# Performance work log

Hardware: AMD Instinct MI355X
Metric: run time of the kernel (lower is better)

Reference implementation:

```python
import jax, jax.numpy as jnp
import numpy as np

EPS = 1e-12  # torch F.normalize eps


def unfold(x, ksize, pad):
    # torch F.unfold equivalent: [B,C,H,W] -> [B, C*k*k, L], channel-major ordering
    patches = jax.lax.conv_general_dilated_patches(
        x, (ksize, ksize), (1, 1), [(pad, pad), (pad, pad)],
        dimension_numbers=('NCHW', 'OIHW', 'NCHW'))
    B, CKK, Hp, Wp = patches.shape
    return patches.reshape(B, CKK, Hp * Wp)


def fold(patches, C, ksize, H, W, pad):
    # torch F.fold equivalent (stride 1): overlap-add of [B, C*k*k, H*W] -> [B,C,H,W]
    B = patches.shape[0]
    p = patches.reshape(B, C, ksize, ksize, H, W)
    out = jnp.zeros((B, C, H + 2 * pad, W + 2 * pad), patches.dtype)
    for di in range(ksize):
        for dj in range(ksize):
            out = out.at[:, :, di:di + H, dj:dj + W].add(p[:, :, di, dj])
    return out[:, :, pad:pad + H, pad:pad + W]


def setup_inputs() -> dict:
    key = jax.random.key(0)
    ks = jax.random.split(key, 4)
    B, C, H, W = 2, 512, 64, 64
    D, CIN = 256, 512 * 9  # embed: Linear(tdim*8*3*3 -> tdim*4), tdim=64
    return {
        'query': jax.random.normal(ks[0], (B, C, H, W), dtype=jnp.float32),
        'key': jax.random.normal(ks[1], (B, C, H, W), dtype=jnp.float32),
        'value': jax.random.normal(ks[2], (B, C, H, W), dtype=jnp.float32),
        'W_embed': jax.random.normal(ks[3], (D, CIN), dtype=jnp.float32) * 0.02,
        'k': 3,
    }


def reference(query, key, value, W_embed, k):
    B, Cv, H, W = value.shape
    # patch embed: unfold -> linear (no bias)
    q_unf = unfold(query, k, k // 2)                       # [B, C*k*k, L]
    k_unf = unfold(key, k, k // 2)                         # [B, C*k*k, L]
    k_emb = jnp.einsum('bcl,dc->bld', k_unf, W_embed)      # [B, L, D]
    q_emb = jnp.einsum('bcl,dc->bdl', q_unf, W_embed)      # [B, D, L]
    # cosine correlation
    k_n = k_emb / jnp.maximum(jnp.linalg.norm(k_emb, axis=2, keepdims=True), EPS)
    q_n = q_emb / jnp.maximum(jnp.linalg.norm(q_emb, axis=1, keepdims=True), EPS)
    corr = jnp.einsum('bld,bdm->blm', k_n, q_n)            # [B, L_key, L_query]
    corr_value = jnp.max(corr, axis=1)                     # [B, L]
    corr_argmax = jnp.argmax(corr, axis=1)                 # [B, L]
    # swap(V=value, idx=corr_argmax, s=1, k=k)
    s = 1
    temph = s * k + H * s - H - s                          # = k - 1
    tempw = s * k + W * s - W - s
    ph = max(temph // 2 + temph % 2, 1)
    pw = max(tempw // 2 + tempw % 2, 1)
    v_unf = unfold(value, k, ph)                           # [B, Cv*k*k, L] (ph==pw for square)
    t_unf = jnp.take_along_axis(v_unf, corr_argmax[:, None, :], axis=2)
    divisor = fold(jnp.ones_like(t_unf), Cv, k, H, W, ph)
    T = fold(t_unf, Cv, k, H, W, ph) / divisor             # [B, Cv, H, W]
    S = corr_value.reshape(B, 1, H, W)
    return S, T
```

## Files before the change

kernel.cpp:

```cpp
#include <hip/hip_runtime.h>
#include <hip/hip_bf16.h>
#include <stdint.h>
#include <math.h>

#define BB 2
#define CC 512
#define HH 64
#define WW 64
#define LL 4096
#define DD 256
#define CIN 4608
#define NG 144

typedef _Float16 half_t;
typedef __attribute__((ext_vector_type(8))) _Float16 f16x8;
typedef __attribute__((ext_vector_type(4))) _Float16 f16x4;
typedef __attribute__((ext_vector_type(4))) float f32x4;

__global__ __launch_bounds__(256) void presplit(const float* __restrict__ query,
                                                const float* __restrict__ key,
                                                char* __restrict__ img_ts) {
    __shared__ float tile[32][65];
    int img = blockIdx.y;
    int y   = blockIdx.x;
    const float* src = ((img >> 1) ? key : query) + (size_t)(img & 1) * CC * LL + y * WW;
    char* dstbase = img_ts + ((size_t)img * 64 + y) * (16 * 64 * 128);
    int t = threadIdx.x;
    int xl = t & 63, c4 = t >> 6;
    int xw = t >> 2, fsw = t & 3;
    for (int cc = 0; cc < 16; ++cc) {
#pragma unroll
        for (int j = 0; j < 8; ++j) {
            int cl = c4 + j * 4;
            tile[cl][xl] = src[(size_t)(cc * 32 + cl) * LL + xl];
        }
        __syncthreads();
        f16x8 h8, l8;
#pragma unroll
        for (int j = 0; j < 8; ++j) {
            float v = tile[fsw * 8 + j][xw];
            half_t h = (half_t)v;
            h8[j] = h; l8[j] = (half_t)(v - (float)h);
        }
        char* p = dstbase + (size_t)cc * 8192 + xw * 128;
        int swz = (xw & 7) << 4;
        *(f16x8*)(p + ((fsw * 16) ^ swz)) = h8;
        *(f16x8*)(p + ((64 + fsw * 16) ^ swz)) = l8;
        __syncthreads();
    }
}

__global__ __launch_bounds__(256) void splitW2b(const float* __restrict__ W,
                                                char* __restrict__ Wst) {
    int i = blockIdx.x * 256 + threadIdx.x;
    if (i >= NG * DD * 4) return;
    int g  = i >> 10;
    int r  = i & 1023;
    int d  = r >> 2;
    int fs = r & 3;
    int cc = g / 9, o = g - cc * 9;
    const float* src = W + (size_t)d * CIN;
    f16x8 h8, l8;
#pragma unroll
    for (int j = 0; j < 8; j++) {
        float w = src[(cc * 32 + fs * 8 + j) * 9 + o];
        half_t h = (half_t)w;
        h8[j] = h;
        l8[j] = (half_t)(w - (float)h);
    }
    size_t base = (size_t)g * 32768 + d * 128;
    int sw = (d & 7) << 4;
    *(f16x8*)(Wst + base + ((fs * 16) ^ sw)) = h8;
    *(f16x8*)(Wst + base + ((64 + fs * 16) ^ sw)) = l8;
}

__global__ __launch_bounds__(512, 2) void embed_mfma(const char* __restrict__ img_ts,
                                                     const char* __restrict__ Wst,
                                                     const char* __restrict__ zp,
                                                     float* __restrict__ part) {
    __shared__ char sW[2][32768];
    __shared__ char sB[2][33792];

    int iid = blockIdx.y;
    int ks  = blockIdx.z;
    int lt  = blockIdx.x;
    int y0  = lt * 2;
    int t = threadIdx.x;
    int w = t >> 6, lane = t & 63;
    int fr = lane & 15, fs = lane >> 4;

    const char* imgb = img_ts + (size_t)iid * (64 * 16 * 64 * 128) + (size_t)ks * 65536;
    const char *ps0, *ps1, *ps2, *ps3, *ps4;
    int pb0, pb1, pb2, pb3, pb4;
#define PREP(qv, PS, PB)                                                \
    {                                                                   \
        int q = (qv);                                                   \
        int ri = q / 528;                                               \
        int rem = q - ri * 528;                                         \
        int xi = rem >> 3, sub = rem & 7;                               \
        int xg = xi - 1, yg = y0 - 1 + ri;                              \
        bool ok = (yg >= 0) && (yg < 64) && (xg >= 0) && (xg < 64);     \
        PS = ok ? imgb + (size_t)yg * 131072 + (size_t)xg * 128 + sub * 16 \
                : zp + ((q & 255) * 16);                                \
        PB = ok ? 8192 : 0;                                             \
    }
    PREP(t, ps0, pb0); PREP(512 + t, ps1, pb1); PREP(1024 + t, ps2, pb2);
    PREP(1536 + t, ps3, pb3); PREP(2048 + t, ps4, pb4);

    const char* pWl = Wst + (size_t)ks * 72 * 32768 + (w << 12) + lane * 16;
    char* wdst0 = &sW[0][0] + (w << 12) + lane * 16;
    char* wdst1 = wdst0 + 32768;
    char* bB0 = &sB[0][0] + t * 16;

    int swzA = (fr & 7) << 4;
    const char* aBH = &sW[0][0] + (w << 12) + fr * 128 + ((fs * 16) ^ swzA);
    const char* aBL = &sW[0][0] + (w << 12) + fr * 128 + ((64 + fs * 16) ^ swzA);
    const char* bH0 = &sB[0][0] + (fr + 0) * 128 + ((fs * 16) ^ (((fr - 1) & 7) << 4));
    const char* bL0 = &sB[0][0] + (fr + 0) * 128 + (((64 + fs * 16)) ^ (((fr - 1) & 7) << 4));
    const char* bH1 = &sB[0][0] + (fr + 1) * 128 + ((fs * 16) ^ (((fr) & 7) << 4));
    const char* bL1 = &sB[0][0] + (fr + 1) * 128 + (((64 + fs * 16)) ^ (((fr) & 7) << 4));
    const char* bH2 = &sB[0][0] + (fr + 2) * 128 + ((fs * 16) ^ (((fr + 1) & 7) << 4));
    const char* bL2 = &sB[0][0] + (fr + 2) * 128 + (((64 + fs * 16)) ^ (((fr + 1) & 7) << 4));

#define GLL(src, dst)                                                   \
    __builtin_amdgcn_global_load_lds(                                   \
        (const __attribute__((address_space(1))) void*)(src),           \
        (__attribute__((address_space(3))) void*)(dst), 16, 0, 0)

#define DMAW(SEL)                                                       \
    do {                                                                \
        char* wd_ = (SEL) ? wdst1 : wdst0;                              \
        GLL(pWl, wd_);                                                  \
        GLL(pWl + 1024, wd_ + 1024);                                    \
        GLL(pWl + 2048, wd_ + 2048);                                    \
        GLL(pWl + 3072, wd_ + 3072);                                    \
        pWl += 32768;                                                   \
    } while (0)

#define DMAB(SEL)                                                       \
    do {                                                                \
        char* bd_ = bB0 + (SEL) * 33792;                                \
        GLL(ps0, bd_);                                                  \
        GLL(ps1, bd_ + 8192);                                           \
        GLL(ps2, bd_ + 16384);                                          \
        GLL(ps3, bd_ + 24576);                                          \
        if (t < 64) GLL(ps4, bd_ + 32768);                              \
        ps0 += pb0; ps1 += pb1; ps2 += pb2; ps3 += pb3; ps4 += pb4;     \
    } while (0)

#define RDA(AH, AL, BSEL)                                               \
    do {                                                                \
        AH[0] = *(const f16x8*)(aBH + (BSEL) * 32768);                  \
        AL[0] = *(const f16x8*)(aBL + (BSEL) * 32768);                  \
        AH[1] = *(const f16x8*)(aBH + 2048 + (BSEL) * 32768);           \
        AL[1] = *(const f16x8*)(aBL + 2048 + (BSEL) * 32768);           \
    } while (0)

#define RDB(DI, DJ, CSEL)                                               \
    do {                                                                \
        const char* h_ = (DJ) == 0 ? bH0 : (DJ) == 1 ? bH1 : bH2;       \
        const char* l_ = (DJ) == 0 ? bL0 : (DJ) == 1 ? bL1 : bL2;       \
        _Pragma("unroll")                                               \
        for (int cg = 0; cg < 8; cg++) {                                \
            int imm = ((cg >> 2) + (DI)) * 8448 + (cg & 3) * 2048 + (CSEL) * 33792; \
            bh[cg] = *(const f16x8*)(h_ + imm);                         \
            bl[cg] = *(const f16x8*)(l_ + imm);                         \
        }                                                               \
    } while (0)

#define DOMFMA(AH, AL)                                                  \
    do {                                                                \
        _Pragma("unroll")                                               \
        for (int rg = 0; rg < 2; rg++)                                  \
            _Pragma("unroll")                                           \
            for (int cg = 0; cg < 8; cg++)                              \
                acc[rg][cg] = __builtin_amdgcn_mfma_f32_16x16x32_f16(AH[rg], bh[cg], acc[rg][cg], 0, 0, 0); \
        _Pragma("unroll")                                               \
        for (int rg = 0; rg < 2; rg++)                                  \
            _Pragma("unroll")                                           \
            for (int cg = 0; cg < 8; cg++) {                            \
                acc[rg][cg] = __builtin_amdgcn_mfma_f32_16x16x32_f16(AH[rg], bl[cg], acc[rg][cg], 0, 0, 0); \
                acc[rg][cg] = __builtin_amdgcn_mfma_f32_16x16x32_f16(AL[rg], bh[cg], acc[rg][cg], 0, 0, 0); \
            }                                                           \
    } while (0)

    f32x4 acc[2][8];
#pragma unroll
    for (int rg = 0; rg < 2; rg++)
#pragma unroll
        for (int cg = 0; cg < 8; cg++) acc[rg][cg] = (f32x4){0.f, 0.f, 0.f, 0.f};

    f16x8 ah0[2], al0[2], ah1[2], al1[2];
    f16x8 bh[8], bl[8];

    DMAB(0);
    DMAW(0);
    DMAW(1);
    asm volatile("s_waitcnt vmcnt(4)" ::: "memory");
    __builtin_amdgcn_sched_barrier(0);
    RDA(ah0, al0, 0);
    __builtin_amdgcn_sched_barrier(0);

#define BODY(KK, O, CSEL, NSEL, DI, DJ)                                 \
    do {                                                                \
        if ((O) == 0) __builtin_amdgcn_s_barrier();                     \
        asm volatile("s_waitcnt lgkmcnt(0)" ::: "memory");              \
        __builtin_amdgcn_sched_barrier(0);                              \
        DMAW((KK) & 1);                                                 \
        if ((O) == 1) DMAB(NSEL);                                       \
        if ((O) == 1 || (O) == 2)                                       \
            asm volatile("s_waitcnt vmcnt(8)" ::: "memory");            \
        else                                                            \
            asm volatile("s_waitcnt vmcnt(4)" ::: "memory");            \
        __builtin_amdgcn_sched_barrier(0);                              \
        if ((KK) & 1) { RDA(ah0, al0, ((KK) + 1) & 1); }                \
        else          { RDA(ah1, al1, ((KK) + 1) & 1); }                \
        RDB(DI, DJ, CSEL);                                              \
        __builtin_amdgcn_sched_barrier(0);                              \
        if ((KK) & 1) DOMFMA(ah1, al1); else DOMFMA(ah0, al0);          \
    } while (0)

#pragma unroll 1
    for (int cp = 0; cp < 4; ++cp) {
        BODY(0, 0, 0, 1, 0, 0);  BODY(1, 1, 0, 1, 0, 1);  BODY(2, 2, 0, 1, 0, 2);
        BODY(3, 3, 0, 1, 1, 0);  BODY(4, 4, 0, 1, 1, 1);  BODY(5, 5, 0, 1, 1, 2);
        BODY(6, 6, 0, 1, 2, 0);  BODY(7, 7, 0, 1, 2, 1);  BODY(8, 8, 0, 1, 2, 2);
        BODY(9, 0, 1, 0, 0, 0);  BODY(10, 1, 1, 0, 0, 1); BODY(11, 2, 1, 0, 0, 2);
        BODY(12, 3, 1, 0, 1, 0); BODY(13, 4, 1, 0, 1, 1); BODY(14, 5, 1, 0, 1, 2);
        BODY(15, 6, 1, 0, 2, 0); BODY(16, 7, 1, 0, 2, 1); BODY(17, 8, 1, 0, 2, 2);
    }
#undef BODY

    float* pt = part + (((size_t)iid * 32 + lt) * 2 + ks) * 32768;
#pragma unroll
    for (int rg = 0; rg < 2; rg++)
#pragma unroll
        for (int cg = 0; cg < 8; cg++) {
            int l = cg * 16 + fr;
            int d0 = w * 32 + rg * 16 + fs * 4;
#pragma unroll
            for (int r = 0; r < 4; r++)
                pt[(d0 + r) * 128 + l] = acc[rg][cg][r];
        }
#undef PREP
#undef GLL
#undef DMAW
#undef DMAB
#undef RDA
#undef RDB
#undef DOMFMA
}

__global__ __launch_bounds__(256) void norm_split(const float* __restrict__ part,
                                                  char* __restrict__ qemb,
                                                  char* __restrict__ kemb) {
    __shared__ float sm[4][64];
    __shared__ float invn[64];
    __shared__ char stage[64][1040];

    int iid = blockIdx.y;
    int bx  = blockIdx.x;
    int lt  = bx >> 1, lh2 = bx & 1;
    const float* p0 = part + (((size_t)iid * 32 + lt) * 2 + 0) * 32768 + lh2 * 64;
    const float* p1 = p0 + 32768;
    int t = threadIdx.x;
    int ll = t & 63, dq = t >> 6;

    float v[64];
    float sq = 0.f;
#pragma unroll
    for (int dd = 0; dd < 64; ++dd) {
        int d = dq * 64 + dd;
        float x = p0[d * 128 + ll] + p1[d * 128 + ll];
        v[dd] = x;
        sq += x * x;
    }
    sm[dq][ll] = sq;
    __syncthreads();
    if (t < 64) {
        float s = sm[0][t] + sm[1][t] + sm[2][t] + sm[3][t];
        invn[t] = 1.0f / fmaxf(sqrtf(s), 1e-12f);
    }
    __syncthreads();

    float sc = invn[ll];
    int swb = (ll & 7) << 4;
#pragma unroll
    for (int oc = 0; oc < 8; ++oc) {
        int d0 = dq * 64 + oc * 8;
        f16x8 h8, l8;
#pragma unroll
        for (int j = 0; j < 8; ++j) {
            float x = v[oc * 8 + j] * sc;
            half_t h = (half_t)x;
            h8[j] = h;
            l8[j] = (half_t)(x - (float)h);
        }
        int itb = d0 >> 5;
        int fsc = (d0 >> 3) & 3;
        *(f16x8*)&stage[ll][itb * 128 + ((fsc * 16) ^ swb)] = h8;
        *(f16x8*)&stage[ll][itb * 128 + ((64 + fsc * 16) ^ swb)] = l8;
    }
    __syncthreads();

    int b = iid & 1, type = iid >> 1;
    char* e = (type ? kemb : qemb);
    int rr = t >> 2, c0 = t & 3;
    char* erow = e + ((size_t)b * LL + lt * 128 + lh2 * 64 + rr) * 1024;
    const char* srow = &stage[rr][0];
#pragma unroll
    for (int c = 0; c < 16; ++c) {
        int cj = c0 + c * 4;
        *(float4*)(erow + cj * 16) = *(const float4*)(srow + cj * 16);
    }
}

__global__ void init_packed(unsigned long long* p, int n) {
    int i = blockIdx.x * 256 + threadIdx.x;
    if (i < n) p[i] = 0ull;
}

__global__ __launch_bounds__(256, 2) void corr_max_mfma(const char* __restrict__ kemb,
                                                        const char* __restrict__ qemb,
                                                        unsigned long long* __restrict__ packed) {
    __shared__ char sA[2][16384];
    __shared__ char sBq[2][16384];

    int b  = blockIdx.z;
    int l0 = blockIdx.y * 128;
    int m0 = blockIdx.x * 128;
    int t  = threadIdx.x;
    int w = t >> 6, lane = t & 63;
    int wr = w >> 1, wc = w & 1;
    int fr = lane & 15, fs = lane >> 4;

    const char* Abase = kemb + ((size_t)b * LL + l0) * 1024;
    const char* Bbase = qemb + ((size_t)b * LL + m0) * 1024;

    f32x4 acc[4][4];
#pragma unroll
    for (int i = 0; i < 4; i++)
#pragma unroll
        for (int j = 0; j < 4; j++) acc[i][j] = (f32x4){0.f, 0.f, 0.f, 0.f};

#define DMA2(bufi, itv)                                                   \
    do {                                                                  \
        _Pragma("unroll")                                                 \
        for (int c = 0; c < 4; c++) {                                     \
            int idx = c * 4096 + t * 16;                                  \
            int row = idx >> 7, offb = idx & 127;                         \
            __builtin_amdgcn_global_load_lds(                             \
                (const __attribute__((address_space(1))) void*)(Abase + (size_t)row * 1024 + (itv) * 128 + offb), \
                (__attribute__((address_space(3))) void*)(&sA[bufi][idx]), 16, 0, 0); \
        }                                                                 \
        _Pragma("unroll")                                                 \
        for (int c = 0; c < 4; c++) {                                     \
            int idx = c * 4096 + t * 16;                                  \
            int row = idx >> 7, offb = idx & 127;                         \
            __builtin_amdgcn_global_load_lds(                             \
                (const __attribute__((address_space(1))) void*)(Bbase + (size_t)row * 1024 + (itv) * 128 + offb), \
                (__attribute__((address_space(3))) void*)(&sBq[bufi][idx]), 16, 0, 0); \
        }                                                                 \
    } while (0)

    DMA2(0, 0);

    f16x8 ah[4], al[4], bh[4], bl[4];
    for (int it = 0; it < 8; ++it) {
        asm volatile("s_waitcnt vmcnt(0) lgkmcnt(0)" ::: "memory");
        __builtin_amdgcn_s_barrier();
        __builtin_amdgcn_sched_barrier(0);
        if (it < 7) DMA2((it + 1) & 1, it + 1);
        __builtin_amdgcn_sched_barrier(0);
        const char* sa = sA[it & 1];
        const char* sb = sBq[it & 1];
#pragma unroll
        for (int rg = 0; rg < 4; rg++) {
            int r = wr * 64 + rg * 16 + fr;
            const char* rp = sa + r * 128;
            int sw_ = (r & 7) << 4;
            ah[rg] = *(const f16x8*)(rp + ((fs * 16) ^ sw_));
            al[rg] = *(const f16x8*)(rp + ((64 + fs * 16) ^ sw_));
        }
#pragma unroll
        for (int cg = 0; cg < 4; cg++) {
            int r = wc * 64 + cg * 16 + fr;
            const char* rp = sb + r * 128;
            int sw_ = (r & 7) << 4;
            bh[cg] = *(const f16x8*)(rp + ((fs * 16) ^ sw_));
            bl[cg] = *(const f16x8*)(rp + ((64 + fs * 16) ^ sw_));
        }
#pragma unroll
        for (int rg = 0; rg < 4; rg++)
#pragma unroll
            for (int cg = 0; cg < 4; cg++)
                acc[rg][cg] = __builtin_amdgcn_mfma_f32_16x16x32_f16(ah[rg], bh[cg], acc[rg][cg], 0, 0, 0);
#pragma unroll
        for (int rg = 0; rg < 4; rg++)
#pragma unroll
            for (int cg = 0; cg < 4; cg++) {
                acc[rg][cg] = __builtin_amdgcn_mfma_f32_16x16x32_f16(ah[rg], bl[cg], acc[rg][cg], 0, 0, 0);
                acc[rg][cg] = __builtin_amdgcn_mfma_f32_16x16x32_f16(al[rg], bh[cg], acc[rg][cg], 0, 0, 0);
            }
    }
#undef DMA2

#pragma unroll
    for (int cg = 0; cg < 4; cg++) {
        unsigned long long best = 0ull;
#pragma unroll
        for (int rg = 0; rg < 4; rg++) {
#pragma unroll
            for (int r = 0; r < 4; r++) {
                unsigned u = __float_as_uint(acc[rg][cg][r]);
                u = (u & 0x80000000u) ? ~u : (u | 0x80000000u);
                int l = l0 + wr * 64 + rg * 16 + fs * 4 + r;
                unsigned long long p = ((unsigned long long)u << 32) | (unsigned)(4095 - l);
                best = (p > best) ? p : best;
            }
        }
        unsigned long long oo;
        oo = __shfl_xor(best, 16); best = (oo > best) ? oo : best;
        oo = __shfl_xor(best, 32); best = (oo > best) ? oo : best;
        if (lane < 16)
            atomicMax(&packed[(size_t)b * LL + m0 + wc * 64 + cg * 16 + lane], best);
    }
}

__global__ void decode_packed(const unsigned long long* __restrict__ packed,
                              float* __restrict__ S_out, int* __restrict__ arg) {
    int i = blockIdx.x * 256 + threadIdx.x;
    if (i < BB * LL) {
        unsigned long long p = packed[i];
        unsigned u = (unsigned)(p >> 32);
        unsigned bits = (u & 0x80000000u) ? (u & 0x7FFFFFFFu) : ~u;
        S_out[i] = __uint_as_float(bits);
        arg[i] = 4095 - (int)(unsigned)(p & 0xFFFFFFFFull);
    }
}

__global__ __launch_bounds__(256) void transpose_mat(const float* __restrict__ src,
                                                     float* __restrict__ dst,
                                                     int R, int Cc) {
    __shared__ float tile[32][33];
    size_t boff = (size_t)blockIdx.z * R * Cc;
    int bx = blockIdx.x;
    int by = blockIdx.y;
    int tx = threadIdx.x & 31;
    int ty = threadIdx.x >> 5;
    const float* s = src + boff;
    float* d = dst + boff;
#pragma unroll
    for (int i = 0; i < 4; i++) {
        int r = by * 32 + ty + i * 8;
        int c = bx * 32 + tx;
        tile[ty + i * 8][tx] = s[(size_t)r * Cc + c];
    }
    __syncthreads();
#pragma unroll
    for (int i = 0; i < 4; i++) {
        int c = bx * 32 + ty + i * 8;
        int r = by * 32 + tx;
        d[(size_t)c * R + r] = tile[tx][ty + i * 8];
    }
}

__global__ __launch_bounds__(256) void gather_fold(const float* __restrict__ value_t,
                                                   const int* __restrict__ arg,
                                                   float* __restrict__ T_t) {
    int b = blockIdx.y;
    int pix = blockIdx.x;
    int y = pix >> 6, x = pix & 63;
    int t = threadIdx.x;
    float2 acc = make_float2(0.f, 0.f);
    int cnty = (y == 0 || y == HH - 1) ? 2 : 3;
    int cntx = (x == 0 || x == WW - 1) ? 2 : 3;
    const int* ab = arg + b * LL;
    const float* vb = value_t + (size_t)b * LL * CC;
#pragma unroll
    for (int di = 0; di < 3; di++) {
        int my = y + 1 - di;
        if (my < 0 || my >= HH) continue;
#pragma unroll
        for (int dj = 0; dj < 3; dj++) {
            int mx = x + 1 - dj;
            if (mx < 0 || mx >= WW) continue;
            int a = ab[my * WW + mx];
            int ay = a >> 6, ax = a & 63;
            int vy = ay + di - 1, vx = ax + dj - 1;
            if (vy < 0 || vy >= HH || vx < 0 || vx >= WW) continue;
            float2 v = *(const float2*)&vb[((size_t)(vy * WW + vx)) * CC + t * 2];
            acc.x += v.x; acc.y += v.y;
        }
    }
    float inv = 1.0f / (float)(cnty * cntx);
    acc.x *= inv; acc.y *= inv;
    *(float2*)&T_t[((size_t)b * LL + pix) * CC + t * 2] = acc;
}

extern "C" void kernel_launch(void* const* d_in, const int* in_sizes, int n_in,
                              void* d_out, int out_size, void* d_ws, size_t ws_size,
                              hipStream_t stream) {
    const float* query = (const float*)d_in[0];
    const float* key   = (const float*)d_in[1];
    const float* value = (const float*)d_in[2];
    const float* Wemb  = (const float*)d_in[3];

    float* out   = (float*)d_out;
    float* S_out = out;
    float* T_out = out + BB * LL;

    char* ws = (char*)d_ws;
    char*  img_ts = ws;
    char*  Wst    = ws + 33554432;
    float* part   = (float*)(ws + 38273024);
    char*  qemb   = ws + 71827456;
    char*  kemb   = ws + 80216064;
    unsigned long long* packed = (unsigned long long*)(ws + 88604672);
    char*  zp     = ws + 88670208;
    int*   arg    = (int*)(ws + 88674304);
    float* val_t  = (float*)(ws + 38273024);
    float* T_t    = (float*)(ws + 38273024 + 16777216);

    init_packed   <<<dim3(34), 256, 0, stream>>>(packed, 8704);
    presplit      <<<dim3(64, 4), 256, 0, stream>>>(query, key, img_ts);
    splitW2b      <<<dim3(576), 256, 0, stream>>>(Wemb, Wst);
    embed_mfma    <<<dim3(32, 4, 2), 512, 0, stream>>>(img_ts, Wst, zp, part);
    norm_split    <<<dim3(64, 4), 256, 0, stream>>>(part, qemb, kemb);
    corr_max_mfma <<<dim3(32, 32, 2), 256, 0, stream>>>(kemb, qemb, packed);
    decode_packed <<<dim3(32), 256, 0, stream>>>(packed, S_out, arg);
    transpose_mat <<<dim3(128, 16, 2), 256, 0, stream>>>(value, val_t, CC, LL);
    gather_fold   <<<dim3(4096, 2), 256, 0, stream>>>(val_t, arg, T_t);
    transpose_mat <<<dim3(16, 128, 2), 256, 0, stream>>>(T_t, T_out, LL, CC);
}
```

Before: 208.5 us.

## Double-buffer B fragments and prefetch LDS reads one step ahead of MFMA

Splits the B-fragment registers into two sets and restructures the GEMM loop so each step issues its MFMAs first, then reads the next step's A/B fragments from LDS and issues the next global-to-LDS DMA. A prologue preloads two steps, and the per-iteration barrier moves to a different step with new wait counts. The goal is to hide LDS read latency behind MFMA work and to remove the full lgkmcnt(0) stall at the start of every step. The cost is doubled B-fragment register use, which may lower occupancy or cause spills. The reworked barrier and vmcnt placement also risks read-before-write hazards on the shared buffers.

```diff
diff --git a/kernel.cpp b/kernel.cpp
--- a/kernel.cpp
+++ b/kernel.cpp
@@ -156,31 +156,31 @@
         AL[1] = *(const f16x8*)(aBL + 2048 + (BSEL) * 32768);           \
     } while (0)
 
-#define RDB(DI, DJ, CSEL)                                               \
+#define RDB(BH, BL, DI, DJ, CSEL)                                       \
     do {                                                                \
         const char* h_ = (DJ) == 0 ? bH0 : (DJ) == 1 ? bH1 : bH2;       \
         const char* l_ = (DJ) == 0 ? bL0 : (DJ) == 1 ? bL1 : bL2;       \
         _Pragma("unroll")                                               \
         for (int cg = 0; cg < 8; cg++) {                                \
             int imm = ((cg >> 2) + (DI)) * 8448 + (cg & 3) * 2048 + (CSEL) * 33792; \
-            bh[cg] = *(const f16x8*)(h_ + imm);                         \
-            bl[cg] = *(const f16x8*)(l_ + imm);                         \
+            BH[cg] = *(const f16x8*)(h_ + imm);                         \
+            BL[cg] = *(const f16x8*)(l_ + imm);                         \
         }                                                               \
     } while (0)
 
-#define DOMFMA(AH, AL)                                                  \
+#define DOMFMA(AH, AL, BH, BL)                                          \
     do {                                                                \
         _Pragma("unroll")                                               \
         for (int rg = 0; rg < 2; rg++)                                  \
             _Pragma("unroll")                                           \
             for (int cg = 0; cg < 8; cg++)                              \
-                acc[rg][cg] = __builtin_amdgcn_mfma_f32_16x16x32_f16(AH[rg], bh[cg], acc[rg][cg], 0, 0, 0); \
+                acc[rg][cg] = __builtin_amdgcn_mfma_f32_16x16x32_f16(AH[rg], BH[cg], acc[rg][cg], 0, 0, 0); \
         _Pragma("unroll")                                               \
         for (int rg = 0; rg < 2; rg++)                                  \
             _Pragma("unroll")                                           \
             for (int cg = 0; cg < 8; cg++) {                            \
-                acc[rg][cg] = __builtin_amdgcn_mfma_f32_16x16x32_f16(AH[rg], bl[cg], acc[rg][cg], 0, 0, 0); \
-                acc[rg][cg] = __builtin_amdgcn_mfma_f32_16x16x32_f16(AL[rg], bh[cg], acc[rg][cg], 0, 0, 0); \
+                acc[rg][cg] = __builtin_amdgcn_mfma_f32_16x16x32_f16(AH[rg], BL[cg], acc[rg][cg], 0, 0, 0); \
+                acc[rg][cg] = __builtin_amdgcn_mfma_f32_16x16x32_f16(AL[rg], BH[cg], acc[rg][cg], 0, 0, 0); \
             }                                                           \
     } while (0)
 
@@ -191,43 +191,70 @@
         for (int cg = 0; cg < 8; cg++) acc[rg][cg] = (f32x4){0.f, 0.f, 0.f, 0.f};
 
     f16x8 ah0[2], al0[2], ah1[2], al1[2];
-    f16x8 bh[8], bl[8];
+    f16x8 bh0[8], bl0[8], bh1[8], bl1[8];
 
     DMAB(0);
     DMAW(0);
     DMAW(1);
     asm volatile("s_waitcnt vmcnt(4)" ::: "memory");
     __builtin_amdgcn_sched_barrier(0);
+    __builtin_amdgcn_s_barrier();
+    __builtin_amdgcn_sched_barrier(0);
     RDA(ah0, al0, 0);
     __builtin_amdgcn_sched_barrier(0);
-
-#define BODY(KK, O, CSEL, NSEL, DI, DJ)                                 \
+    RDB(bh0, bl0, 0, 0, 0);
+    asm volatile("s_waitcnt lgkmcnt(15)" ::: "memory");
+    __builtin_amdgcn_sched_barrier(0);
+    DMAW(0);
+    asm volatile("s_waitcnt vmcnt(4)" ::: "memory");
+    __builtin_amdgcn_sched_barrier(0);
+    RDA(ah1, al1, 1);
+    __builtin_amdgcn_sched_barrier(0);
+    RDB(bh1, bl1, 0, 1, 0);
+    asm volatile("s_waitcnt lgkmcnt(15)" ::: "memory");
+    __builtin_amdgcn_sched_barrier(0);
+    DMAW(1);
+
+#define BODY(KK, O, CSEL2, DI2, DJ2, V8)                                \
     do {                                                                \
-        if ((O) == 0) __builtin_amdgcn_s_barrier();                     \
-        asm volatile("s_waitcnt lgkmcnt(0)" ::: "memory");              \
-        __builtin_amdgcn_sched_barrier(0);                              \
-        DMAW((KK) & 1);                                                 \
-        if ((O) == 1) DMAB(NSEL);                                       \
-        if ((O) == 1 || (O) == 2)                                       \
+        if ((O) == 7) {                                                 \
+            asm volatile("s_waitcnt lgkmcnt(0)" ::: "memory");          \
+            __builtin_amdgcn_s_barrier();                               \
+            __builtin_amdgcn_sched_barrier(0);                          \
+        }                                                               \
+        if ((KK) >= 15)                                                 \
+            asm volatile("s_waitcnt vmcnt(0)" ::: "memory");            \
+        else if (V8)                                                    \
             asm volatile("s_waitcnt vmcnt(8)" ::: "memory");            \
         else                                                            \
             asm volatile("s_waitcnt vmcnt(4)" ::: "memory");            \
         __builtin_amdgcn_sched_barrier(0);                              \
-        if ((KK) & 1) { RDA(ah0, al0, ((KK) + 1) & 1); }                \
-        else          { RDA(ah1, al1, ((KK) + 1) & 1); }                \
-        RDB(DI, DJ, CSEL);                                              \
+        if ((KK) & 1) DOMFMA(ah1, al1, bh1, bl1);                       \
+        else          DOMFMA(ah0, al0, bh0, bl0);                       \
         __builtin_amdgcn_sched_barrier(0);                              \
-        if ((KK) & 1) DOMFMA(ah1, al1); else DOMFMA(ah0, al0);          \
+        if (cp < 3 || (KK) < 16) {                                      \
+            if ((KK) & 1) { RDA(ah1, al1, (KK) & 1);                    \
+                            __builtin_amdgcn_sched_barrier(0);          \
+                            RDB(bh1, bl1, DI2, DJ2, CSEL2); }           \
+            else          { RDA(ah0, al0, (KK) & 1);                    \
+                            __builtin_amdgcn_sched_barrier(0);          \
+                            RDB(bh0, bl0, DI2, DJ2, CSEL2); }           \
+        }                                                               \
+        asm volatile("s_waitcnt lgkmcnt(15)" ::: "memory");             \
+        __builtin_amdgcn_sched_barrier(0);                              \
+        if (cp < 3 || (KK) < 14) DMAW((KK) & 1);                        \
+        if ((O) == 1) { if ((KK) == 1 || cp < 3) DMAB(((KK) == 1) ? 1 : 0); } \
+        __builtin_amdgcn_sched_barrier(0);                              \
     } while (0)
 
 #pragma unroll 1
     for (int cp = 0; cp < 4; ++cp) {
-        BODY(0, 0, 0, 1, 0, 0);  BODY(1, 1, 0, 1, 0, 1);  BODY(2, 2, 0, 1, 0, 2);
-        BODY(3, 3, 0, 1, 1, 0);  BODY(4, 4, 0, 1, 1, 1);  BODY(5, 5, 0, 1, 1, 2);
-        BODY(6, 6, 0, 1, 2, 0);  BODY(7, 7, 0, 1, 2, 1);  BODY(8, 8, 0, 1, 2, 2);
-        BODY(9, 0, 1, 0, 0, 0);  BODY(10, 1, 1, 0, 0, 1); BODY(11, 2, 1, 0, 0, 2);
-        BODY(12, 3, 1, 0, 1, 0); BODY(13, 4, 1, 0, 1, 1); BODY(14, 5, 1, 0, 1, 2);
-        BODY(15, 6, 1, 0, 2, 0); BODY(16, 7, 1, 0, 2, 1); BODY(17, 8, 1, 0, 2, 2);
+        BODY(0, 0, 0, 0, 2, 0);  BODY(1, 1, 0, 1, 0, 0);  BODY(2, 2, 0, 1, 1, 1);
+        BODY(3, 3, 0, 1, 2, 1);  BODY(4, 4, 0, 2, 0, 0);  BODY(5, 5, 0, 2, 1, 0);
+        BODY(6, 6, 0, 2, 2, 0);  BODY(7, 7, 1, 0, 0, 0);  BODY(8, 8, 1, 0, 1, 0);
+        BODY(9, 0, 1, 0, 2, 0);  BODY(10, 1, 1, 1, 0, 0); BODY(11, 2, 1, 1, 1, 1);
+        BODY(12, 3, 1, 1, 2, 1); BODY(13, 4, 1, 2, 0, 0); BODY(14, 5, 1, 2, 1, 0);
+        BODY(15, 6, 1, 2, 2, 0); BODY(16, 7, 0, 0, 0, 0); BODY(17, 8, 0, 0, 1, 0);
     }
 #undef BODY
 
```

Measured after the change: 261.1 us. 25.2% more time.

## Fuse gather-fold with output transpose and parallelize presplit over channel chunks

Applied to the files above, without the earlier changes.

The gather/fold kernel now writes the channel-major output directly through a shared-memory staging tile, which removes the intermediate T_t buffer and the final transpose kernel. Each block handles one row, 128 channels and one batch, precomputing the source pixel indices and inverse divisors in shared memory. The presplit kernel is spread across a third grid dimension over the 16 channel chunks, giving 4096 blocks instead of 256 to fill the GPU better. The fused gather has each lane reading single floats with a stride along channels, and the grid has only 512 blocks, so coalescing and occupancy may be worse than before.

```diff
diff --git a/kernel.cpp b/kernel.cpp
--- a/kernel.cpp
+++ b/kernel.cpp
@@ -21,33 +21,31 @@
                                                 const float* __restrict__ key,
                                                 char* __restrict__ img_ts) {
     __shared__ float tile[32][65];
-    int img = blockIdx.y;
     int y   = blockIdx.x;
+    int cc  = blockIdx.y;
+    int img = blockIdx.z;
     const float* src = ((img >> 1) ? key : query) + (size_t)(img & 1) * CC * LL + y * WW;
     char* dstbase = img_ts + ((size_t)img * 64 + y) * (16 * 64 * 128);
     int t = threadIdx.x;
     int xl = t & 63, c4 = t >> 6;
     int xw = t >> 2, fsw = t & 3;
-    for (int cc = 0; cc < 16; ++cc) {
-#pragma unroll
-        for (int j = 0; j < 8; ++j) {
-            int cl = c4 + j * 4;
-            tile[cl][xl] = src[(size_t)(cc * 32 + cl) * LL + xl];
-        }
-        __syncthreads();
-        f16x8 h8, l8;
-#pragma unroll
-        for (int j = 0; j < 8; ++j) {
-            float v = tile[fsw * 8 + j][xw];
-            half_t h = (half_t)v;
-            h8[j] = h; l8[j] = (half_t)(v - (float)h);
-        }
-        char* p = dstbase + (size_t)cc * 8192 + xw * 128;
-        int swz = (xw & 7) << 4;
-        *(f16x8*)(p + ((fsw * 16) ^ swz)) = h8;
-        *(f16x8*)(p + ((64 + fsw * 16) ^ swz)) = l8;
-        __syncthreads();
-    }
+#pragma unroll
+    for (int j = 0; j < 8; ++j) {
+        int cl = c4 + j * 4;
+        tile[cl][xl] = src[(size_t)(cc * 32 + cl) * LL + xl];
+    }
+    __syncthreads();
+    f16x8 h8, l8;
+#pragma unroll
+    for (int j = 0; j < 8; ++j) {
+        float v = tile[fsw * 8 + j][xw];
+        half_t h = (half_t)v;
+        h8[j] = h; l8[j] = (half_t)(v - (float)h);
+    }
+    char* p = dstbase + (size_t)cc * 8192 + xw * 128;
+    int swz = (xw & 7) << 4;
+    *(f16x8*)(p + ((fsw * 16) ^ swz)) = h8;
+    *(f16x8*)(p + ((64 + fsw * 16) ^ swz)) = l8;
 }
 
 __global__ __launch_bounds__(256) void splitW2b(const float* __restrict__ W,
@@ -465,37 +463,65 @@
     }
 }
 
-__global__ __launch_bounds__(256) void gather_fold(const float* __restrict__ value_t,
-                                                   const int* __restrict__ arg,
-                                                   float* __restrict__ T_t) {
-    int b = blockIdx.y;
-    int pix = blockIdx.x;
-    int y = pix >> 6, x = pix & 63;
-    int t = threadIdx.x;
-    float2 acc = make_float2(0.f, 0.f);
-    int cnty = (y == 0 || y == HH - 1) ? 2 : 3;
-    int cntx = (x == 0 || x == WW - 1) ? 2 : 3;
-    const int* ab = arg + b * LL;
-    const float* vb = value_t + (size_t)b * LL * CC;
-#pragma unroll
-    for (int di = 0; di < 3; di++) {
-        int my = y + 1 - di;
-        if (my < 0 || my >= HH) continue;
-#pragma unroll
-        for (int dj = 0; dj < 3; dj++) {
-            int mx = x + 1 - dj;
-            if (mx < 0 || mx >= WW) continue;
-            int a = ab[my * WW + mx];
+__global__ __launch_bounds__(256) void gather_fold_t(const float* __restrict__ val_t,
+                                                     const int* __restrict__ arg,
+                                                     float* __restrict__ T_out) {
+    __shared__ int srcpix[64][9];
+    __shared__ float invw[64];
+    __shared__ float stage[32][65];
+
+    int y  = blockIdx.x;
+    int cq = blockIdx.y;
+    int b  = blockIdx.z;
+    int t  = threadIdx.x;
+
+    if (t < 64) {
+        int x = t;
+        int cnty = (y == 0 || y == HH - 1) ? 2 : 3;
+        int cntx = (x == 0 || x == WW - 1) ? 2 : 3;
+        invw[x] = 1.0f / (float)(cnty * cntx);
+    }
+    for (int e = t; e < 576; e += 256) {
+        int x = e / 9, r = e - x * 9;
+        int di = r / 3, dj = r - di * 3;
+        int my = y + 1 - di, mx = x + 1 - dj;
+        int s = -1;
+        if (my >= 0 && my < HH && mx >= 0 && mx < WW) {
+            int a = arg[b * LL + my * WW + mx];
             int ay = a >> 6, ax = a & 63;
             int vy = ay + di - 1, vx = ax + dj - 1;
-            if (vy < 0 || vy >= HH || vx < 0 || vx >= WW) continue;
-            float2 v = *(const float2*)&vb[((size_t)(vy * WW + vx)) * CC + t * 2];
-            acc.x += v.x; acc.y += v.y;
-        }
-    }
-    float inv = 1.0f / (float)(cnty * cntx);
-    acc.x *= inv; acc.y *= inv;
-    *(float2*)&T_t[((size_t)b * LL + pix) * CC + t * 2] = acc;
+            if (vy >= 0 && vy < HH && vx >= 0 && vx < WW) s = vy * WW + vx;
+        }
+        srcpix[x][r] = s;
+    }
+    __syncthreads();
+
+    const float* vb = val_t + (size_t)b * LL * CC;
+    int cl = t & 31;
+    int xq = t >> 5;
+    int xl = t & 63;
+    for (int s4 = 0; s4 < 4; ++s4) {
+        int c = cq * 128 + s4 * 32 + cl;
+#pragma unroll
+        for (int p = 0; p < 8; ++p) {
+            int x = xq + p * 8;
+            float acc = 0.f;
+#pragma unroll
+            for (int r = 0; r < 9; ++r) {
+                int s = srcpix[x][r];
+                if (s >= 0) acc += vb[(size_t)s * CC + c];
+            }
+            stage[cl][x] = acc * invw[x];
+        }
+        __syncthreads();
+        float* To = T_out + ((size_t)b * CC + cq * 128 + s4 * 32) * LL + y * WW;
+#pragma unroll
+        for (int j = 0; j < 8; ++j) {
+            int cw = (t >> 6) + j * 4;
+            To[(size_t)cw * LL + xl] = stage[cw][xl];
+        }
+        __syncthreads();
+    }
 }
 
 extern "C" void kernel_launch(void* const* d_in, const int* in_sizes, int n_in,
@@ -520,16 +546,14 @@
     char*  zp     = ws + 88670208;
     int*   arg    = (int*)(ws + 88674304);
     float* val_t  = (float*)(ws + 38273024);
-    float* T_t    = (float*)(ws + 38273024 + 16777216);
 
     init_packed   <<<dim3(34), 256, 0, stream>>>(packed, 8704);
-    presplit      <<<dim3(64, 4), 256, 0, stream>>>(query, key, img_ts);
+    presplit      <<<dim3(64, 16, 4), 256, 0, stream>>>(query, key, img_ts);
     splitW2b      <<<dim3(576), 256, 0, stream>>>(Wemb, Wst);
     embed_mfma    <<<dim3(32, 4, 2), 512, 0, stream>>>(img_ts, Wst, zp, part);
     norm_split    <<<dim3(64, 4), 256, 0, stream>>>(part, qemb, kemb);
     corr_max_mfma <<<dim3(32, 32, 2), 256, 0, stream>>>(kemb, qemb, packed);
     decode_packed <<<dim3(32), 256, 0, stream>>>(packed, S_out, arg);
     transpose_mat <<<dim3(128, 16, 2), 256, 0, stream>>>(value, val_t, CC, LL);
-    gather_fold   <<<dim3(4096, 2), 256, 0, stream>>>(val_t, arg, T_t);
-    transpose_mat <<<dim3(16, 128, 2), 256, 0, stream>>>(T_t, T_out, LL, CC);
-}
+    gather_fold_t <<<dim3(64, 4, 2), 256, 0, stream>>>(val_t, arg, T_out);
+}
```

After: 272.1 us. +30.5%, slower.
